# Performance work log

Hardware: AMD Instinct MI355X
Metric: run time of the kernel (lower is better)

Reference implementation:

```python
import jax, jax.numpy as jnp
import numpy as np

K_PERIODS = 4   # k_periods
PMAX = 64       # pmax
MIN_P = 16      # min_period_threshold (already clamped to <= PMAX)


def setup_inputs() -> dict:
    key = jax.random.key(0)
    B, T, N = 32, 512, 128
    x = jax.random.normal(key, (B, T, N), dtype=jnp.float32)
    return {"x": x}


def reference(x):
    # x: [B, T, N]
    B, T, N = x.shape
    K = K_PERIODS
    seqs = jnp.transpose(x, (0, 2, 1)).reshape(B * N, T)  # [BN, T]

    # top-k nonzero frequencies by rFFT amplitude
    spec = jnp.fft.rfft(seqs, axis=-1)                    # [BN, T//2+1]
    amp = jnp.abs(spec)
    amp = amp.at[..., 0].set(0.0)                         # zero DC component
    kamp, kidx = jax.lax.top_k(amp, K)                    # [BN, K] each
    kidx = jnp.maximum(kidx, 1)

    # periods and cycle counts
    P = jnp.clip(T // kidx, MIN_P, PMAX)                  # [BN, K]
    cycles = jnp.maximum(T // P, 1)                       # [BN, K]
    take = cycles * P

    # static upper bound on cycles (torch uses data-dependent cycles.max();
    # extra trailing cycle slots here are fully masked to zero)
    Cmax = T // MIN_P
    idx_c = jnp.arange(Cmax)                              # [Cmax]
    idx_p = jnp.arange(PMAX)                              # [Pmax]

    base = jnp.maximum(T - take, 0)[..., None, None]      # [BN, K, 1, 1]
    indices = base + idx_c[None, None, :, None] * P[..., None, None] \
              + idx_p[None, None, None, :]                # [BN, K, Cmax, Pmax]
    indices = jnp.clip(indices, 0, T - 1)

    # gather: broadcast seqs over (K, Cmax)
    gathered = jnp.take_along_axis(seqs[:, None, None, :], indices, axis=-1)

    mask = ((idx_c[None, None, :, None] < cycles[..., None, None]) &
            (idx_p[None, None, None, :] < P[..., None, None])).astype(x.dtype)
    gathered = gathered * mask

    gathered = gathered.reshape(B, N, K, Cmax, PMAX)
    mask = mask.reshape(B, N, K, Cmax, PMAX)
    kamp = kamp.reshape(B, N, K)
    return gathered, mask, kamp
```

## Files before the change

kernel.cpp:

```cpp
#include <hip/hip_runtime.h>
#include <math.h>

#define TLEN 512
#define NCH  128
#define KP   4
#define PMAXV 64
#define CMAXV 32
#define MINP 16
#define NSEQ 4096
#define OUTG ((size_t)NSEQ * KP * CMAXV * PMAXV)

#define PAD8(i) ((i) + ((i) >> 3))
#define XP   580
#define SEQP 520

typedef float nfloat4 __attribute__((ext_vector_type(4)));

__global__ __launch_bounds__(256) void periodicity_kernel(
    const float* __restrict__ x,
    float* __restrict__ out_g,
    float* __restrict__ out_m,
    float* __restrict__ out_a)
{
    const int tid  = threadIdx.x;
    const int lane = tid & 63;
    const int w    = tid >> 6;
    const int s0   = blockIdx.x << 2;
    const int b    = s0 >> 7;
    const int n0   = s0 & (NCH - 1);

    __shared__ float   seqf[4 * SEQP];
    __shared__ double  re[4 * XP];
    __shared__ double  im[4 * XP];
    __shared__ double2 W[256];

    {
        const int col = tid & 3;
        const int t0  = tid >> 2;
        const float* base = x + (size_t)b * TLEN * NCH + n0 + col;
        #pragma unroll
        for (int it = 0; it < 8; ++it) {
            const int t = t0 + 64 * it;
            seqf[col * SEQP + t] = base[(size_t)t * NCH];
        }
        double ang = -6.283185307179586476925286766559 * (double)tid / (double)TLEN;
        double sv, cv;
        sincos(ang, &sv, &cv);
        W[tid] = make_double2(cv, sv);
    }
    __syncthreads();

    float*  sf = seqf + w * SEQP;
    double* RE = re + w * XP;
    double* IM = im + w * XP;

    #pragma unroll
    for (int u = 0; u < 8; ++u) {
        const int i = lane + 64 * u;
        const int r = (int)(__brev((unsigned)i) >> 23);
        RE[PAD8(i)] = (double)sf[r];
        IM[PAD8(i)] = 0.0;
    }
    __builtin_amdgcn_wave_barrier();

    for (int st = 1; st <= 9; ++st) {
        const int half = 1 << (st - 1);
        #pragma unroll
        for (int u = 0; u < 4; ++u) {
            const int j   = lane + 64 * u;
            const int pos = j & (half - 1);
            const int i1  = ((j >> (st - 1)) << st) + pos;
            const int i2  = i1 + half;
            const double2 wv = W[pos << (9 - st)];
            const double ar = RE[PAD8(i1)], ai = IM[PAD8(i1)];
            const double cr = RE[PAD8(i2)], ci = IM[PAD8(i2)];
            const double tr = wv.x * cr - wv.y * ci;
            const double ti = wv.x * ci + wv.y * cr;
            RE[PAD8(i1)] = ar + tr;  IM[PAD8(i1)] = ai + ti;
            RE[PAD8(i2)] = ar - tr;  IM[PAD8(i2)] = ai - ti;
        }
        __builtin_amdgcn_wave_barrier();
    }

    double a[5];
    int    bins[5];
    #pragma unroll
    for (int u = 0; u < 4; ++u) {
        const int k = lane + 64 * u;
        const double xr = RE[PAD8(k)], xi = IM[PAD8(k)];
        a[u]    = (k == 0) ? 0.0 : (xr * xr + xi * xi);
        bins[u] = k;
    }
    a[4]    = -1.0;
    bins[4] = 256;
    if (lane == 0) {
        const double xr = RE[PAD8(256)], xi = IM[PAD8(256)];
        a[4] = xr * xr + xi * xi;
    }

    double bv0, bv1, bv2, bv3;
    int    bi0, bi1, bi2, bi3;
    #pragma unroll
    for (int q = 0; q < KP; ++q) {
        double v  = a[0];
        int    vi = bins[0];
        #pragma unroll
        for (int j = 1; j < 5; ++j)
            if (a[j] > v) { v = a[j]; vi = bins[j]; }
        #pragma unroll
        for (int off = 32; off > 0; off >>= 1) {
            const double ov = __shfl_xor(v, off, 64);
            const int    oi = __shfl_xor(vi, off, 64);
            if (ov > v || (ov == v && oi < vi)) { v = ov; vi = oi; }
        }
        if (q == 0) { bv0 = v; bi0 = vi; }
        else if (q == 1) { bv1 = v; bi1 = vi; }
        else if (q == 2) { bv2 = v; bi2 = vi; }
        else { bv3 = v; bi3 = vi; }
        #pragma unroll
        for (int j = 0; j < 5; ++j)
            if (bins[j] == vi) a[j] = -1.0;
    }

    int P0, P1, P2, P3, C0, C1, C2, C3, B0, B1, B2, B3;
    {
        int k0 = bi0 < 1 ? 1 : bi0;  P0 = TLEN / k0;
        P0 = P0 < MINP ? MINP : (P0 > PMAXV ? PMAXV : P0);
        C0 = TLEN / P0;  B0 = TLEN - C0 * P0;
        int k1 = bi1 < 1 ? 1 : bi1;  P1 = TLEN / k1;
        P1 = P1 < MINP ? MINP : (P1 > PMAXV ? PMAXV : P1);
        C1 = TLEN / P1;  B1 = TLEN - C1 * P1;
        int k2 = bi2 < 1 ? 1 : bi2;  P2 = TLEN / k2;
        P2 = P2 < MINP ? MINP : (P2 > PMAXV ? PMAXV : P2);
        C2 = TLEN / P2;  B2 = TLEN - C2 * P2;
        int k3 = bi3 < 1 ? 1 : bi3;  P3 = TLEN / k3;
        P3 = P3 < MINP ? MINP : (P3 > PMAXV ? PMAXV : P3);
        C3 = TLEN / P3;  B3 = TLEN - C3 * P3;
    }
    const int s = s0 + w;
    if (lane == 0) {
        out_a[(size_t)s * KP + 0] = (float)sqrt(bv0);
        out_a[(size_t)s * KP + 1] = (float)sqrt(bv1);
        out_a[(size_t)s * KP + 2] = (float)sqrt(bv2);
        out_a[(size_t)s * KP + 3] = (float)sqrt(bv3);
    }

    float* og = out_g + (size_t)s * (KP * CMAXV * PMAXV);
    float* om = out_m + (size_t)s * (KP * CMAXV * PMAXV);
    const int pp = (lane & 15) << 2;

    for (int r = lane >> 4; r < KP * CMAXV; r += 4) {
        const int k = r >> 5;
        const int c = r & (CMAXV - 1);
        const int P    = k == 0 ? P0 : k == 1 ? P1 : k == 2 ? P2 : P3;
        const int cyc  = k == 0 ? C0 : k == 1 ? C1 : k == 2 ? C2 : C3;
        nfloat4 m = (nfloat4)(0.f, 0.f, 0.f, 0.f);
        if (c < cyc) {
            m.x = (pp     < P) ? 1.f : 0.f;
            m.y = (pp + 1 < P) ? 1.f : 0.f;
            m.z = (pp + 2 < P) ? 1.f : 0.f;
            m.w = (pp + 3 < P) ? 1.f : 0.f;
        }
        *(nfloat4*)(om + r * PMAXV + pp) = m;
    }

    for (int r = lane >> 4; r < KP * CMAXV; r += 4) {
        const int k = r >> 5;
        const int c = r & (CMAXV - 1);
        const int P    = k == 0 ? P0 : k == 1 ? P1 : k == 2 ? P2 : P3;
        const int cyc  = k == 0 ? C0 : k == 1 ? C1 : k == 2 ? C2 : C3;
        const int base = k == 0 ? B0 : k == 1 ? B1 : k == 2 ? B2 : B3;
        nfloat4 g = (nfloat4)(0.f, 0.f, 0.f, 0.f);
        if (c < cyc) {
            const int idx = base + c * P + pp;
            if (pp     < P) g.x = sf[idx];
            if (pp + 1 < P) g.y = sf[idx + 1];
            if (pp + 2 < P) g.z = sf[idx + 2];
            if (pp + 3 < P) g.w = sf[idx + 3];
        }
        *(nfloat4*)(og + r * PMAXV + pp) = g;
    }
}

extern "C" void kernel_launch(void* const* d_in, const int* in_sizes, int n_in,
                              void* d_out, int out_size, void* d_ws, size_t ws_size,
                              hipStream_t stream) {
    const float* x = (const float*)d_in[0];
    float* out = (float*)d_out;
    float* og = out;
    float* om = out + OUTG;
    float* oa = om + OUTG;

    periodicity_kernel<<<dim3(NSEQ / 4), dim3(256), 0, stream>>>(x, og, om, oa);
}
```

Before: 273.2 us.

## Compute real FFT via half-length complex FFT with post-processing twiddle

Packs the 512 real samples as 256 complex values and runs a 256-point radix-2 FFT, then recovers the real-input spectrum with the standard even/odd split and twiddle step. This halves the butterfly stages' work and the shared-memory traffic, and stores complex values as interleaved double2. The cost is an extra post-processing pass with paired reads at k and 256-k. The kernel is likely dominated by the output writes, so the effect on total time may be limited.

```diff
diff --git a/kernel.cpp b/kernel.cpp
--- a/kernel.cpp
+++ b/kernel.cpp
@@ -11,7 +11,7 @@
 #define OUTG ((size_t)NSEQ * KP * CMAXV * PMAXV)
 
 #define PAD8(i) ((i) + ((i) >> 3))
-#define XP   580
+#define ZP   290
 #define SEQP 520
 
 typedef float nfloat4 __attribute__((ext_vector_type(4)));
@@ -30,8 +30,7 @@
     const int n0   = s0 & (NCH - 1);
 
     __shared__ float   seqf[4 * SEQP];
-    __shared__ double  re[4 * XP];
-    __shared__ double  im[4 * XP];
+    __shared__ double2 Z[4 * ZP];
     __shared__ double2 W[256];
 
     {
@@ -50,63 +49,71 @@
     }
     __syncthreads();
 
-    float*  sf = seqf + w * SEQP;
-    double* RE = re + w * XP;
-    double* IM = im + w * XP;
+    float*   sf = seqf + w * SEQP;
+    double2* Zw = Z + w * ZP;
 
     #pragma unroll
-    for (int u = 0; u < 8; ++u) {
+    for (int u = 0; u < 4; ++u) {
         const int i = lane + 64 * u;
-        const int r = (int)(__brev((unsigned)i) >> 23);
-        RE[PAD8(i)] = (double)sf[r];
-        IM[PAD8(i)] = 0.0;
+        const int r = (int)(__brev((unsigned)i) >> 24);
+        const float2 p = ((const float2*)sf)[r];
+        Zw[PAD8(i)] = make_double2((double)p.x, (double)p.y);
     }
     __builtin_amdgcn_wave_barrier();
 
-    for (int st = 1; st <= 9; ++st) {
+    for (int st = 1; st <= 8; ++st) {
         const int half = 1 << (st - 1);
         #pragma unroll
-        for (int u = 0; u < 4; ++u) {
+        for (int u = 0; u < 2; ++u) {
             const int j   = lane + 64 * u;
             const int pos = j & (half - 1);
             const int i1  = ((j >> (st - 1)) << st) + pos;
             const int i2  = i1 + half;
             const double2 wv = W[pos << (9 - st)];
-            const double ar = RE[PAD8(i1)], ai = IM[PAD8(i1)];
-            const double cr = RE[PAD8(i2)], ci = IM[PAD8(i2)];
-            const double tr = wv.x * cr - wv.y * ci;
-            const double ti = wv.x * ci + wv.y * cr;
-            RE[PAD8(i1)] = ar + tr;  IM[PAD8(i1)] = ai + ti;
-            RE[PAD8(i2)] = ar - tr;  IM[PAD8(i2)] = ai - ti;
+            const double2 a  = Zw[PAD8(i1)];
+            const double2 c  = Zw[PAD8(i2)];
+            const double tr = wv.x * c.x - wv.y * c.y;
+            const double ti = wv.x * c.y + wv.y * c.x;
+            Zw[PAD8(i1)] = make_double2(a.x + tr, a.y + ti);
+            Zw[PAD8(i2)] = make_double2(a.x - tr, a.y - ti);
         }
         __builtin_amdgcn_wave_barrier();
     }
 
-    double a[5];
+    double av[5];
     int    bins[5];
     #pragma unroll
     for (int u = 0; u < 4; ++u) {
         const int k = lane + 64 * u;
-        const double xr = RE[PAD8(k)], xi = IM[PAD8(k)];
-        a[u]    = (k == 0) ? 0.0 : (xr * xr + xi * xi);
+        const double2 zk = Zw[PAD8(k)];
+        const double2 zm = Zw[PAD8((256 - k) & 255)];
+        const double gr = 0.5 * (zk.x + zm.x);
+        const double gi = 0.5 * (zk.y - zm.y);
+        const double hr = 0.5 * (zk.y + zm.y);
+        const double hi = 0.5 * (zm.x - zk.x);
+        const double2 wv = W[k];
+        const double xr = gr + wv.x * hr - wv.y * hi;
+        const double xi = gi + wv.x * hi + wv.y * hr;
+        av[u]   = (k == 0) ? 0.0 : (xr * xr + xi * xi);
         bins[u] = k;
     }
-    a[4]    = -1.0;
+    av[4]   = -1.0;
     bins[4] = 256;
     if (lane == 0) {
-        const double xr = RE[PAD8(256)], xi = IM[PAD8(256)];
-        a[4] = xr * xr + xi * xi;
+        const double2 z0 = Zw[PAD8(0)];
+        const double nyq = z0.x - z0.y;
+        av[4] = nyq * nyq;
     }
 
     double bv0, bv1, bv2, bv3;
     int    bi0, bi1, bi2, bi3;
     #pragma unroll
     for (int q = 0; q < KP; ++q) {
-        double v  = a[0];
+        double v  = av[0];
         int    vi = bins[0];
         #pragma unroll
         for (int j = 1; j < 5; ++j)
-            if (a[j] > v) { v = a[j]; vi = bins[j]; }
+            if (av[j] > v) { v = av[j]; vi = bins[j]; }
         #pragma unroll
         for (int off = 32; off > 0; off >>= 1) {
             const double ov = __shfl_xor(v, off, 64);
@@ -119,7 +126,7 @@
         else { bv3 = v; bi3 = vi; }
         #pragma unroll
         for (int j = 0; j < 5; ++j)
-            if (bins[j] == vi) a[j] = -1.0;
+            if (bins[j] == vi) av[j] = -1.0;
     }
 
     int P0, P1, P2, P3, C0, C1, C2, C3, B0, B1, B2, B3;
@@ -152,8 +159,8 @@
     for (int r = lane >> 4; r < KP * CMAXV; r += 4) {
         const int k = r >> 5;
         const int c = r & (CMAXV - 1);
-        const int P    = k == 0 ? P0 : k == 1 ? P1 : k == 2 ? P2 : P3;
-        const int cyc  = k == 0 ? C0 : k == 1 ? C1 : k == 2 ? C2 : C3;
+        const int P   = k == 0 ? P0 : k == 1 ? P1 : k == 2 ? P2 : P3;
+        const int cyc = k == 0 ? C0 : k == 1 ? C1 : k == 2 ? C2 : C3;
         nfloat4 m = (nfloat4)(0.f, 0.f, 0.f, 0.f);
         if (c < cyc) {
             m.x = (pp     < P) ? 1.f : 0.f;
```

After: 269.5 us. Within noise of the previous version (-1.3%).
